# Kernel tuning notes

Hardware: AMD Instinct MI355X
Metric: run time of the kernel (lower is better)

The kernel has to match this reference:

```python
import jax, jax.numpy as jnp
import numpy as np

N, L, H, E, FE = 32, 128, 16, 256, 4  # batch, seq_len, heads, embed_size, forward_expansion
EPS = 1e-5
NEG_SLOPE = 0.01


def _mask_positions(qe):
    # zero entries where j < L-1-i (torch: triu(ones,1).flip(1) == 1)
    Ld = qe.shape[-1]
    i = jnp.arange(Ld)[:, None]
    j = jnp.arange(Ld)[None, :]
    return jnp.where(j >= (Ld - 1 - i), qe, jnp.zeros((), qe.dtype))


def _skew(qe):
    # pad last dim on the left, reinterpret, drop first row -> relative skew
    n, h, Ld, _ = qe.shape
    p = jnp.pad(qe, ((0, 0), (0, 0), (0, 0), (1, 0)))
    return p.reshape(n, h, Ld + 1, Ld)[:, :, 1:, :]


def _batchnorm(x, gamma, beta):
    # BatchNorm1d(C=L*H) over (N, C, E): normalize over batch and embed dims
    mean = jnp.mean(x, axis=(0, 2), keepdims=True)
    var = jnp.var(x, axis=(0, 2), keepdims=True)
    return (x - mean) * jax.lax.rsqrt(var + EPS) * gamma[None, :, None] + beta[None, :, None]


def _leaky(x):
    return jnp.where(x >= 0, x, NEG_SLOPE * x)


def setup_inputs() -> dict:
    key = jax.random.key(0)
    ks = jax.random.split(key, 16)
    s_e = 1.0 / np.sqrt(E)
    d = {
        "x": jax.random.normal(ks[0], (N, L * H, E, 1), dtype=jnp.float32),
        "Wq": jax.random.normal(ks[1], (E, E), dtype=jnp.float32) * s_e,
        "bq": jnp.zeros((E,), jnp.float32),
        "Wk": jax.random.normal(ks[2], (E, E), dtype=jnp.float32) * s_e,
        "bk": jnp.zeros((E,), jnp.float32),
        "Wv": jax.random.normal(ks[3], (E, E), dtype=jnp.float32) * s_e,
        "bv": jnp.zeros((E,), jnp.float32),
        "Erel": jax.random.normal(ks[4], (H, L, E), dtype=jnp.float32),
        "Wo": jax.random.normal(ks[5], (E, E), dtype=jnp.float32) * s_e,
        "bo": jnp.zeros((E,), jnp.float32),
        "g1": jnp.ones((L * H,), jnp.float32),
        "be1": jnp.zeros((L * H,), jnp.float32),
        "g2": jnp.ones((L * H,), jnp.float32),
        "be2": jnp.zeros((L * H,), jnp.float32),
        "W1": jax.random.normal(ks[6], (E, FE * E), dtype=jnp.float32) * s_e,
        "b1": jnp.zeros((FE * E,), jnp.float32),
        "W2": jax.random.normal(ks[7], (FE * E, E), dtype=jnp.float32) * (1.0 / np.sqrt(FE * E)),
        "b2": jnp.zeros((E,), jnp.float32),
        "Wenc": jax.random.normal(ks[8], (E, E), dtype=jnp.float32) * s_e,
        "benc": jnp.zeros((E,), jnp.float32),
    }
    return d


def reference(x, Wq, bq, Wk, bk, Wv, bv, Erel, Wo, bo, g1, be1, g2, be2, W1, b1, W2, b2, Wenc, benc):
    xs = x[:, :, :, 0]  # (N, L*H, E)
    q = (xs @ Wq + bq).reshape(N, L, H, E)
    k = (xs @ Wk + bk).reshape(N, L, H, E)
    v = (xs @ Wv + bv).reshape(N, L, H, E)
    # relative-position skew term (Music-Transformer style)
    QE = jnp.einsum('nlhe,hme->nhlm', q, Erel)       # (N,H,L,L)
    S = _skew(_mask_positions(QE))                   # (N,H,L,L)
    qk = jnp.einsum('nqhe,nkhe->nhqk', q, k)         # (N,H,L,L)
    att = jax.nn.softmax(qk / jnp.sqrt(jnp.float32(E)), axis=-1) + S
    z = jnp.einsum('nhql,nlhe->nqhe', att, v).reshape(N, L * H, E)
    z = z @ Wo + bo
    h1 = _batchnorm(z + xs, g1, be1)
    ff = _leaky(h1 @ W1 + b1) @ W2 + b2
    out = _batchnorm(ff + h1, g2, be2)
    return out @ Wenc + benc
```

## Files before the change

### kernel.cpp

```cpp
#include <hip/hip_runtime.h>
#include <hip/hip_bf16.h>

using u16 = unsigned short;
typedef __attribute__((ext_vector_type(8))) short bf16x8;
typedef __attribute__((ext_vector_type(4))) float f32x4;

static constexpr float EPS_ = 1e-5f;
static constexpr float NEG_ = 0.01f;

__device__ __forceinline__ float bf2f(u16 u) { return __uint_as_float(((unsigned)u) << 16); }
__device__ __forceinline__ u16 f2bf(float f) {
    union { __hip_bfloat16 h; u16 u; } c; c.h = __float2bfloat16(f); return c.u;
}

#define MFMA16(a, b, c) __builtin_amdgcn_mfma_f32_16x16x32_bf16(a, b, c, 0, 0, 0)

__device__ __forceinline__ void gload16(const u16* g, u16* l) {
    __builtin_amdgcn_global_load_lds(
        (__attribute__((address_space(1))) void*)(u16*)g,
        (__attribute__((address_space(3))) void*)l, 16, 0, 0);
}

__device__ __forceinline__ int xswz(int nwg) {
    const int b = blockIdx.x;
    return (b & 7) * (nwg >> 3) + (b >> 3);
}

template<int K>
__device__ __forceinline__ void core256(
    const u16* __restrict__ Ag, int lda,
    const u16* __restrict__ Bg, int ldb,
    u16* SH, f32x4 acc[8][4])
{
    const int tid = threadIdx.x;
    const int w = tid >> 6, lane = tid & 63;
    const int g = lane >> 4, r = lane & 15;
    const int wr = w >> 2, wc = w & 3;
    const int gx = (g ^ ((r >> 1) & 3)) * 8;
    constexpr int NT = K / 32;

    #pragma unroll
    for (int i = 0; i < 8; i++)
        #pragma unroll
        for (int j = 0; j < 4; j++)
            acc[i][j] = (f32x4){0.f, 0.f, 0.f, 0.f};

    auto stage = [&](int buf, int kt, int rnd) {
        const int part = rnd & 1, isB = rnd >> 1;
        const int u = part * 512 + tid;
        const int row = u >> 2;
        const int sc = (u & 3) ^ ((row >> 1) & 3);
        const u16* src = (isB ? Bg + (size_t)row * ldb : Ag + (size_t)row * lda)
                         + kt + sc * 8;
        gload16(src, SH + buf * 16384 + isB * 8192 + u * 8);
    };

    #pragma unroll
    for (int rnd = 0; rnd < 4; ++rnd) stage(0, 0, rnd);
    asm volatile("s_waitcnt vmcnt(0)" ::: "memory");
    __builtin_amdgcn_s_barrier();
    __builtin_amdgcn_sched_barrier(0);

    for (int t = 0; t < NT; ++t) {
        const int buf = t & 1;
        const u16* Ab = SH + buf * 16384;
        const u16* Bb = Ab + 8192;
        const bool pf = (t + 1 < NT);

        if (pf) { stage(buf ^ 1, (t + 1) * 32, 0); stage(buf ^ 1, (t + 1) * 32, 1); }
        bf16x8 bfr[4], af[4];
        #pragma unroll
        for (int fn = 0; fn < 4; ++fn)
            bfr[fn] = *(const bf16x8*)(Bb + (wc * 64 + fn * 16 + r) * 32 + gx);
        #pragma unroll
        for (int f = 0; f < 4; ++f)
            af[f] = *(const bf16x8*)(Ab + (wr * 128 + f * 16 + r) * 32 + gx);
        __builtin_amdgcn_s_setprio(1);
        #pragma unroll
        for (int f = 0; f < 4; ++f)
            #pragma unroll
            for (int fn = 0; fn < 4; ++fn)
                acc[f][fn] = MFMA16(af[f], bfr[fn], acc[f][fn]);
        __builtin_amdgcn_s_setprio(0);

        if (pf) { stage(buf ^ 1, (t + 1) * 32, 2); stage(buf ^ 1, (t + 1) * 32, 3); }
        #pragma unroll
        for (int f = 0; f < 4; ++f)
            af[f] = *(const bf16x8*)(Ab + (wr * 128 + 64 + f * 16 + r) * 32 + gx);
        __builtin_amdgcn_s_setprio(1);
        #pragma unroll
        for (int f = 0; f < 4; ++f)
            #pragma unroll
            for (int fn = 0; fn < 4; ++fn)
                acc[4 + f][fn] = MFMA16(af[f], bfr[fn], acc[4 + f][fn]);
        __builtin_amdgcn_s_setprio(0);

        asm volatile("s_waitcnt vmcnt(0)" ::: "memory");
        __builtin_amdgcn_s_barrier();
        __builtin_amdgcn_sched_barrier(0);
    }
}

template<int K, int NN, int MODE>
__global__ __launch_bounds__(512, 2) void gemm256_k(
    const u16* __restrict__ A, const u16* __restrict__ Bt,
    const float* __restrict__ bias, const u16* __restrict__ res,
    const float2* __restrict__ rp, const float* __restrict__ cs,
    void* __restrict__ outv)
{
    __shared__ __align__(16) u16 SH[36864];
    constexpr int NB = NN / 256;
    const int f = xswz(256 * NB);
    const int m0 = (f / NB) * 256, n0 = (f % NB) * 256;

    f32x4 acc[8][4];
    core256<K>(A + (size_t)m0 * K, K, Bt + (size_t)n0 * K, K, SH, acc);

    const int tid = threadIdx.x;
    const int w = tid >> 6, lane = tid & 63;
    const int g = lane >> 4, r = lane & 15;
    const int wr = w >> 2, wc = w & 3;

    __syncthreads();

    if constexpr (MODE == 3) {
        float* SHf = (float*)SH;
        float* out = (float*)outv;
        #pragma unroll
        for (int q = 0; q < 4; ++q) {
            if (wr == (q >> 1)) {
                const int fmB = (q & 1) * 4;
                #pragma unroll
                for (int fi = 0; fi < 4; ++fi) {
                    #pragma unroll
                    for (int fn = 0; fn < 4; ++fn) {
                        const int col = wc * 64 + fn * 16 + r;
                        const float bv = bias[n0 + col], cv = cs[n0 + col];
                        #pragma unroll
                        for (int reg = 0; reg < 4; ++reg) {
                            const int rl = fi * 16 + g * 4 + reg;
                            const int m = m0 + q * 64 + rl;
                            const float2 pp = rp[m & 2047];
                            SHf[rl * 260 + col] =
                                pp.x * acc[fmB + fi][fn][reg] + pp.y * cv + bv;
                        }
                    }
                }
            }
            __builtin_amdgcn_s_barrier();
            #pragma unroll
            for (int p = 0; p < 8; ++p) {
                const int id = p * 512 + tid;
                const int rl = id >> 6, c4 = id & 63;
                const float4 v = *(const float4*)(SHf + rl * 260 + c4 * 4);
                *(float4*)(out + (size_t)(m0 + q * 64 + rl) * 256 + c4 * 4) = v;
            }
            __builtin_amdgcn_s_barrier();
        }
        return;
    }

    u16* out = (u16*)outv;
    #pragma unroll
    for (int h = 0; h < 2; ++h) {
        if (wr == h) {
            #pragma unroll
            for (int fm = 0; fm < 8; ++fm)
                #pragma unroll
                for (int fn = 0; fn < 4; ++fn) {
                    const int col = wc * 64 + fn * 16 + r;
                    const float bv = bias[n0 + col];
                    #pragma unroll
                    for (int reg = 0; reg < 4; ++reg) {
                        const int rl = fm * 16 + g * 4 + reg;
                        float v = acc[fm][fn][reg];
                        if constexpr (MODE == 1) {
                            const float2 pp = rp[(m0 + h * 128 + rl) & 2047];
                            v = pp.x * v + pp.y * cs[n0 + col] + bv;
                            v = v >= 0.f ? v : NEG_ * v;
                        } else {
                            v += bv;
                        }
                        SH[rl * 264 + col] = f2bf(v);
                    }
                }
        }
        __builtin_amdgcn_s_barrier();
        #pragma unroll
        for (int p = 0; p < 8; ++p) {
            const int ck = p * 512 + tid;
            const int rl = ck >> 5, cc = ck & 31;
            const int m = m0 + h * 128 + rl;
            bf16x8 v = *(const bf16x8*)(SH + rl * 264 + cc * 8);
            if constexpr (MODE == 0) {
                const bf16x8 rv = *(const bf16x8*)(res + (size_t)m * NN + n0 + cc * 8);
                #pragma unroll
                for (int j = 0; j < 8; ++j)
                    v[j] = (short)f2bf(bf2f((u16)v[j]) + bf2f((u16)rv[j]));
            }
            if constexpr (MODE == 2) {
                const float2 pp = rp[m & 2047];
                const bf16x8 rv = *(const bf16x8*)(res + (size_t)m * NN + n0 + cc * 8);
                #pragma unroll
                for (int j = 0; j < 8; ++j)
                    v[j] = (short)f2bf(bf2f((u16)v[j]) + pp.x * bf2f((u16)rv[j]) + pp.y);
            }
            *(bf16x8*)(out + (size_t)m * NN + n0 + cc * 8) = v;
        }
        __builtin_amdgcn_s_barrier();
    }
}

__global__ __launch_bounds__(512, 2) void qkv256_k(
    const u16* __restrict__ xbf, const u16* __restrict__ Wqkvt,
    const float* __restrict__ bq, const float* __restrict__ bk,
    const float* __restrict__ bv,
    u16* __restrict__ qo, u16* __restrict__ ko, u16* __restrict__ vo)
{
    __shared__ __align__(16) u16 SH[36864];
    const int f = xswz(768);
    const int m0 = (f / 3) * 256;
    const int which = f % 3;
    const float* bias = which == 0 ? bq : (which == 1 ? bk : bv);

    f32x4 acc[8][4];
    core256<256>(xbf + (size_t)m0 * 256, 256,
                 Wqkvt + (size_t)which * 65536, 256, SH, acc);

    const int tid = threadIdx.x;
    const int w = tid >> 6, lane = tid & 63;
    const int g = lane >> 4, r = lane & 15;
    const int wr = w >> 2, wc = w & 3;
    const int nn = m0 >> 11;

    __syncthreads();
    if (which < 2) {
        u16* out = which == 0 ? qo : ko;
        #pragma unroll
        for (int h = 0; h < 2; ++h) {
            if (wr == h) {
                #pragma unroll
                for (int fm = 0; fm < 8; ++fm)
                    #pragma unroll
                    for (int fn = 0; fn < 4; ++fn) {
                        const int col = wc * 64 + fn * 16 + r;
                        const float bv4 = bias[col];
                        #pragma unroll
                        for (int reg = 0; reg < 4; ++reg) {
                            const int rl = fm * 16 + g * 4 + reg;
                            SH[rl * 264 + col] = f2bf(acc[fm][fn][reg] + bv4);
                        }
                    }
            }
            __builtin_amdgcn_s_barrier();
            #pragma unroll
            for (int p = 0; p < 8; ++p) {
                const int ck = p * 512 + tid;
                const int rl = ck >> 5, cc = ck & 31;
                const int m = m0 + h * 128 + rl;
                const int l = (m & 2047) >> 4, hh = m & 15;
                const bf16x8 v = *(const bf16x8*)(SH + rl * 264 + cc * 8);
                *(bf16x8*)(out + ((size_t)(nn * 16 + hh) * 128 + l) * 256 + cc * 8) = v;
            }
            __builtin_amdgcn_s_barrier();
        }
    } else {
        #pragma unroll
        for (int h = 0; h < 2; ++h) {
            if (wr == h) {
                #pragma unroll
                for (int fm = 0; fm < 8; ++fm)
                    #pragma unroll
                    for (int fn = 0; fn < 4; ++fn) {
                        const int col = wc * 64 + fn * 16 + r;
                        const float bv4 = bias[col];
                        #pragma unroll
                        for (int reg = 0; reg < 4; ++reg) {
                            const int rl = fm * 16 + g * 4 + reg;
                            SH[col * 136 + ((rl & 15) * 8 | (rl >> 4))] =
                                f2bf(acc[fm][fn][reg] + bv4);
                        }
                    }
            }
            __builtin_amdgcn_s_barrier();
            const int l0 = ((m0 + h * 128) & 2047) >> 4;
            #pragma unroll
            for (int p = 0; p < 8; ++p) {
                const int ck = p * 512 + tid;
                const int e = ck >> 4, hh = ck & 15;
                const bf16x8 v = *(const bf16x8*)(SH + e * 136 + hh * 8);
                *(bf16x8*)(vo + ((size_t)(nn * 16 + hh) * 256 + e) * 128 + l0) = v;
            }
            __builtin_amdgcn_s_barrier();
        }
    }
}

__device__ __forceinline__ void lds_core(
    const u16* __restrict__ Ag, int lda,
    const u16* __restrict__ Bg, int ldb, int K,
    u16* As, u16* Bs, f32x4 acc[4][4])
{
    const int tid = threadIdx.x;
    const int w = tid >> 6, lane = tid & 63;
    const int g = lane >> 4, r = lane & 15;
    const int wm = (w >> 1) * 64, wn = (w & 1) * 64;
    const int rx = r & 7;

    for (int kt = 0; kt < K; kt += 64) {
        #pragma unroll
        for (int j = 0; j < 4; j++) {
            const int ubase = (w * 4 + j) * 64;
            const int u = ubase + lane;
            const int row = u >> 3;
            const int cb = ((u & 7) ^ (row & 7)) * 8;
            gload16(Ag + (size_t)row * lda + kt + cb, As + ubase * 8);
            gload16(Bg + (size_t)row * ldb + kt + cb, Bs + ubase * 8);
        }
        __syncthreads();
        #pragma unroll
        for (int kk = 0; kk < 2; kk++) {
            const int co = ((kk * 4 + g) ^ rx) * 8;
            bf16x8 af[4], bfr[4];
            #pragma unroll
            for (int f = 0; f < 4; f++) {
                af[f]  = *(const bf16x8*)(As + (wm + f * 16 + r) * 64 + co);
                bfr[f] = *(const bf16x8*)(Bs + (wn + f * 16 + r) * 64 + co);
            }
            #pragma unroll
            for (int i = 0; i < 4; i++)
                #pragma unroll
                for (int j = 0; j < 4; j++)
                    acc[i][j] = MFMA16(af[i], bfr[j], acc[i][j]);
        }
        __syncthreads();
    }
}

template<typename OutF>
__device__ __forceinline__ void epi_store128(
    u16* Cs, f32x4 (&acc)[4][4], float scale, OutF outp)
{
    const int tid = threadIdx.x;
    const int w = tid >> 6, lane = tid & 63;
    const int g = lane >> 4, r = lane & 15;
    const int mb = (w >> 1) * 64, nb = (w & 1) * 64;

    #pragma unroll
    for (int fn = 0; fn < 4; fn++) {
        const int col = nb + fn * 16 + r;
        #pragma unroll
        for (int fm = 0; fm < 4; fm++)
            #pragma unroll
            for (int reg = 0; reg < 4; reg++) {
                const int row = mb + fm * 16 + g * 4 + reg;
                Cs[row * 136 + col] = f2bf(acc[fm][fn][reg] * scale);
            }
    }
    __syncthreads();
    #pragma unroll
    for (int p = 0; p < 8; p++) {
        const int ck = p * 256 + tid;
        const int row = ck >> 4, cc = ck & 15;
        const bf16x8 v = *(const bf16x8*)(Cs + row * 136 + cc * 8);
        *(bf16x8*)outp(row, cc) = v;
    }
}

__global__ __launch_bounds__(256) void qkqe_k(
    const u16* __restrict__ q, const u16* __restrict__ kc,
    const u16* __restrict__ erel, u16* __restrict__ out)
{
    __shared__ __align__(16) u16 SH[17408];
    u16* As = SH; u16* Bs = SH + 8192;
    const int f = xswz(1024);
    const int b = f >> 1, h = b & 15;
    const int n0 = (f & 1) * 128;
    const u16* Ag = q + (size_t)b * 128 * 256;
    const u16* Bg = (n0 == 0) ? (kc + (size_t)b * 128 * 256)
                              : (erel + (size_t)h * 128 * 256);

    f32x4 acc[4][4];
    #pragma unroll
    for (int i = 0; i < 4; i++)
        #pragma unroll
        for (int j = 0; j < 4; j++) acc[i][j] = (f32x4){0.f,0.f,0.f,0.f};
    lds_core(Ag, 256, Bg, 256, 256, As, Bs, acc);

    const float scale = (n0 == 0) ? 0.0625f : 1.0f;
    __syncthreads();
    epi_store128(SH, acc, scale,
        [&](int row, int cc) -> u16* {
            return out + ((size_t)b * 128 + row) * 256 + n0 + cc * 8;
        });
}

__global__ __launch_bounds__(256) void softmax_k(
    const u16* __restrict__ qk, u16* __restrict__ att)
{
    const int r = blockIdx.x * 4 + (threadIdx.x >> 6);
    const int lane = threadIdx.x & 63;
    const int i = r & 127;
    const u16* row = qk + (size_t)r * 256;
    const float x0 = bf2f(row[lane]), x1 = bf2f(row[lane + 64]);
    float mx = fmaxf(x0, x1);
    #pragma unroll
    for (int o = 32; o; o >>= 1) mx = fmaxf(mx, __shfl_xor(mx, o));
    const float e0 = __expf(x0 - mx), e1 = __expf(x1 - mx);
    float s = e0 + e1;
    #pragma unroll
    for (int o = 32; o; o >>= 1) s += __shfl_xor(s, o);
    const float rinv = 1.0f / s;
    const float s0 = (lane <= i) ? bf2f(row[128 + 127 - i + lane]) : 0.f;
    const float s1 = (lane + 64 <= i) ? bf2f(row[128 + 127 - i + lane + 64]) : 0.f;
    att[(size_t)r * 128 + lane] = f2bf(e0 * rinv + s0);
    att[(size_t)r * 128 + lane + 64] = f2bf(e1 * rinv + s1);
}

__global__ __launch_bounds__(256) void av_k(
    const u16* __restrict__ att, const u16* __restrict__ vT,
    u16* __restrict__ zc)
{
    __shared__ __align__(16) u16 SH[17408];
    u16* As = SH; u16* Bs = SH + 8192;
    const int f = xswz(1024);
    const int b = f >> 1;
    const int n0 = (f & 1) * 128;
    const u16* Ag = att + (size_t)b * 128 * 128;
    const u16* Bg = vT + (size_t)b * 256 * 128 + (size_t)n0 * 128;

    f32x4 acc[4][4];
    #pragma unroll
    for (int i = 0; i < 4; i++)
        #pragma unroll
        for (int j = 0; j < 4; j++) acc[i][j] = (f32x4){0.f,0.f,0.f,0.f};
    lds_core(Ag, 128, Bg, 128, 128, As, Bs, acc);

    const int nn = b >> 4, hh = b & 15;
    __syncthreads();
    epi_store128(SH, acc, 1.f,
        [&](int row, int cc) -> u16* {
            return zc + ((size_t)(nn * 2048 + row * 16 + hh)) * 256 + n0 + cc * 8;
        });
}

__global__ __launch_bounds__(256) void cvt_k(const float* __restrict__ in,
                                             u16* __restrict__ out) {
    const size_t i8 = ((size_t)blockIdx.x * 256 + threadIdx.x) * 8;
    const float4 lo = *(const float4*)(in + i8);
    const float4 hi = *(const float4*)(in + i8 + 4);
    ushort4 o0, o1;
    o0.x = f2bf(lo.x); o0.y = f2bf(lo.y); o0.z = f2bf(lo.z); o0.w = f2bf(lo.w);
    o1.x = f2bf(hi.x); o1.y = f2bf(hi.y); o1.z = f2bf(hi.z); o1.w = f2bf(hi.w);
    *(ushort4*)(out + i8) = o0;
    *(ushort4*)(out + i8 + 4) = o1;
}

__global__ __launch_bounds__(256) void prep_w_k(
    const float* __restrict__ Wq, const float* __restrict__ Wk,
    const float* __restrict__ Wv, const float* __restrict__ Wo,
    const float* __restrict__ Wenc, const float* __restrict__ W1,
    const float* __restrict__ W2, const float* __restrict__ Erel,
    u16* __restrict__ Wqkvt, u16* __restrict__ Wot, u16* __restrict__ Wenct,
    u16* __restrict__ W1t, u16* __restrict__ W2t, u16* __restrict__ Erelb,
    float* __restrict__ cs1, float* __restrict__ csE)
{
    const int bid = blockIdx.x, tid = threadIdx.x;
    if (bid < 1280) {
        const int jb = bid >> 8;
        const int t = ((bid & 255) << 8) | tid;
        const int n = t >> 8, k = t & 255;
        const float* src = jb == 0 ? Wq : jb == 1 ? Wk : jb == 2 ? Wv
                         : jb == 3 ? Wo : Wenc;
        const u16 v = f2bf(src[(k << 8) + n]);
        if (jb < 3)       Wqkvt[jb * 65536 + t] = v;
        else if (jb == 3) Wot[t] = v;
        else              Wenct[t] = v;
    } else if (bid < 2304) {
        const int t = ((bid - 1280) << 8) | tid;
        const int n = t >> 8, k = t & 255;
        W1t[t] = f2bf(W1[(k << 10) + n]);
    } else if (bid < 3328) {
        const int t = ((bid - 2304) << 8) | tid;
        const int n = t >> 10, k = t & 1023;
        W2t[t] = f2bf(W2[(k << 8) + n]);
    } else if (bid < 5376) {
        const int t = ((bid - 3328) << 8) | tid;
        Erelb[t] = f2bf(Erel[t]);
    } else {
        const int n = (bid - 5376) * 256 + tid;
        if (n < 1024) {
            float s = 0.f;
            for (int k = 0; k < 256; ++k) s += bf2f(f2bf(W1[(size_t)k * 1024 + n]));
            cs1[n] = s;
        } else {
            const int n2 = n - 1024;
            float s = 0.f;
            for (int k = 0; k < 256; ++k) s += bf2f(f2bf(Wenc[(size_t)k * 256 + n2]));
            csE[n2] = s;
        }
    }
}

__global__ __launch_bounds__(256) void bnstats_k(
    const u16* __restrict__ x, const float* __restrict__ g,
    const float* __restrict__ be, float2* __restrict__ params)
{
    const int c = blockIdx.x, tid = threadIdx.x;
    float s = 0.f, s2 = 0.f;
    #pragma unroll 4
    for (int n = 0; n < 32; n++) {
        const float v = bf2f(x[((size_t)n * 2048 + c) * 256 + tid]);
        s += v; s2 += v * v;
    }
    #pragma unroll
    for (int o = 32; o; o >>= 1) { s += __shfl_xor(s, o); s2 += __shfl_xor(s2, o); }
    __shared__ float rs[4], rs2[4];
    const int w = tid >> 6;
    if ((tid & 63) == 0) { rs[w] = s; rs2[w] = s2; }
    __syncthreads();
    if (tid == 0) {
        s  = rs[0] + rs[1] + rs[2] + rs[3];
        s2 = rs2[0] + rs2[1] + rs2[2] + rs2[3];
        const float mean = s / 8192.f;
        const float var = s2 / 8192.f - mean * mean;
        const float a = g[c] * rsqrtf(var + EPS_);
        params[c] = make_float2(a, be[c] - mean * a);
    }
}

extern "C" void kernel_launch(void* const* d_in, const int* in_sizes, int n_in,
                              void* d_out, int out_size, void* d_ws, size_t ws_size,
                              hipStream_t stream)
{
    const float* x    = (const float*)d_in[0];
    const float* Wq   = (const float*)d_in[1];
    const float* bq   = (const float*)d_in[2];
    const float* Wk   = (const float*)d_in[3];
    const float* bk   = (const float*)d_in[4];
    const float* Wv   = (const float*)d_in[5];
    const float* bv   = (const float*)d_in[6];
    const float* Erel = (const float*)d_in[7];
    const float* Wo   = (const float*)d_in[8];
    const float* bo   = (const float*)d_in[9];
    const float* g1   = (const float*)d_in[10];
    const float* be1  = (const float*)d_in[11];
    const float* g2   = (const float*)d_in[12];
    const float* be2  = (const float*)d_in[13];
    const float* W1   = (const float*)d_in[14];
    const float* b1   = (const float*)d_in[15];
    const float* W2   = (const float*)d_in[16];
    const float* b2   = (const float*)d_in[17];
    const float* Wenc = (const float*)d_in[18];
    const float* benc = (const float*)d_in[19];

    char* ws = (char*)d_ws;
    const size_t MB = 1ull << 20;
    const size_t KB = 1024;
    u16* xbf   = (u16*)(ws + 0 * MB);
    u16* h2pre = (u16*)(ws + 32 * MB);
    u16* qb    = (u16*)(ws + 32 * MB);
    u16* kb    = (u16*)(ws + 64 * MB);
    u16* vT    = (u16*)(ws + 96 * MB);
    u16* qkb   = (u16*)(ws + 128 * MB);
    u16* attb  = (u16*)(ws + 160 * MB);
    u16* ff1   = (u16*)(ws + 64 * MB);
    u16* zc    = (u16*)(ws + 176 * MB);
    u16* h1pre = (u16*)(ws + 208 * MB);
    u16* Wqkvt = (u16*)(ws + 240 * MB);
    u16* Wot   = (u16*)(ws + 240 * MB + 512 * KB);
    u16* Wenct = (u16*)(ws + 240 * MB + 640 * KB);
    u16* W1t   = (u16*)(ws + 240 * MB + 768 * KB);
    u16* W2t   = (u16*)(ws + 240 * MB + 1280 * KB);
    u16* Erelb = (u16*)(ws + 240 * MB + 1792 * KB);
    float2* p1 = (float2*)(ws + 243 * MB);
    float2* p2 = (float2*)(ws + 243 * MB + 16 * KB);
    float* cs1 = (float*)(ws + 243 * MB + 32 * KB);
    float* csE = (float*)(ws + 243 * MB + 40 * KB);

    const dim3 b256(256), b512(512);

    cvt_k<<<dim3(8192), b256, 0, stream>>>(x, xbf);
    prep_w_k<<<dim3(5381), b256, 0, stream>>>(Wq, Wk, Wv, Wo, Wenc, W1, W2, Erel,
                                              Wqkvt, Wot, Wenct, W1t, W2t, Erelb,
                                              cs1, csE);

    qkv256_k<<<dim3(768), b512, 0, stream>>>(xbf, Wqkvt, bq, bk, bv, qb, kb, vT);
    qkqe_k<<<dim3(1024), b256, 0, stream>>>(qb, kb, Erelb, qkb);
    softmax_k<<<dim3(16384), b256, 0, stream>>>(qkb, attb);
    av_k<<<dim3(1024), b256, 0, stream>>>(attb, vT, zc);
    gemm256_k<256, 256, 0><<<dim3(256), b512, 0, stream>>>(
        zc, Wot, bo, xbf, nullptr, nullptr, h1pre);

    bnstats_k<<<dim3(2048), b256, 0, stream>>>(h1pre, g1, be1, p1);

    gemm256_k<256, 1024, 1><<<dim3(1024), b512, 0, stream>>>(
        h1pre, W1t, b1, nullptr, p1, cs1, ff1);
    gemm256_k<1024, 256, 2><<<dim3(256), b512, 0, stream>>>(
        ff1, W2t, b2, h1pre, p1, nullptr, h2pre);

    bnstats_k<<<dim3(2048), b256, 0, stream>>>(h2pre, g2, be2, p2);
    gemm256_k<256, 256, 3><<<dim3(256), b512, 0, stream>>>(
        h2pre, Wenct, benc, nullptr, p2, csE, (float*)d_out);
}
```

Before: 337.1 us.

## Deepen GEMM core pipeline to 64-wide K steps with two-stage prefetch

The shared 256x256 GEMM core now processes K in 64-element steps split into two 32-wide halves. Loads for the next halves are issued two stages ahead, and partial vmcnt waits replace the full drain before each barrier. The LDS swizzle changes to match the new layout. LDS per block grows to 128 KB and the launch bounds drop the two-blocks-per-CU hint, so occupancy likely falls to one 512-thread block per CU in exchange for more latency hiding.

```diff
diff --git a/kernel.cpp b/kernel.cpp
--- a/kernel.cpp
+++ b/kernel.cpp
@@ -36,8 +36,8 @@
     const int w = tid >> 6, lane = tid & 63;
     const int g = lane >> 4, r = lane & 15;
     const int wr = w >> 2, wc = w & 3;
-    const int gx = (g ^ ((r >> 1) & 3)) * 8;
-    constexpr int NT = K / 32;
+    const int gx = (g ^ (r & 3)) * 8;
+    constexpr int NT = K / 64;
 
     #pragma unroll
     for (int i = 0; i < 8; i++)
@@ -45,36 +45,46 @@
         for (int j = 0; j < 4; j++)
             acc[i][j] = (f32x4){0.f, 0.f, 0.f, 0.f};
 
-    auto stage = [&](int buf, int kt, int rnd) {
-        const int part = rnd & 1, isB = rnd >> 1;
-        const int u = part * 512 + tid;
-        const int row = u >> 2;
-        const int sc = (u & 3) ^ ((row >> 1) & 3);
-        const u16* src = (isB ? Bg + (size_t)row * ldb : Ag + (size_t)row * lda)
-                         + kt + sc * 8;
-        gload16(src, SH + buf * 16384 + isB * 8192 + u * 8);
+    auto stage_half = [&](int Tt, int which) {
+        const int isB = which & 1, kh = which >> 1;
+        const int d2 = Tt & 1;
+        u16* base = SH + (size_t)((d2 * 2 + isB) * 2 + kh) * 8192;
+        const u16* gbase = isB ? Bg : Ag;
+        const int ld = isB ? ldb : lda;
+        const int kt = Tt * 64 + kh * 32;
+        #pragma unroll
+        for (int part = 0; part < 2; ++part) {
+            const int u = part * 512 + tid;
+            const int row = u >> 2;
+            const int gslot = (u & 3) ^ (row & 3);
+            gload16(gbase + (size_t)row * ld + kt + gslot * 8, base + u * 8);
+        }
     };
 
-    #pragma unroll
-    for (int rnd = 0; rnd < 4; ++rnd) stage(0, 0, rnd);
-    asm volatile("s_waitcnt vmcnt(0)" ::: "memory");
-    __builtin_amdgcn_s_barrier();
-    __builtin_amdgcn_sched_barrier(0);
+    stage_half(0, 0); stage_half(0, 1); stage_half(0, 2); stage_half(0, 3);
+    stage_half(1, 0); stage_half(1, 1);
 
     for (int t = 0; t < NT; ++t) {
-        const int buf = t & 1;
-        const u16* Ab = SH + buf * 16384;
-        const u16* Bb = Ab + 8192;
-        const bool pf = (t + 1 < NT);
-
-        if (pf) { stage(buf ^ 1, (t + 1) * 32, 0); stage(buf ^ 1, (t + 1) * 32, 1); }
-        bf16x8 bfr[4], af[4];
+        const int d = t & 1;
+        const u16* Ak0 = SH + (size_t)(d * 4 + 0) * 8192;
+        const u16* Ak1 = SH + (size_t)(d * 4 + 1) * 8192;
+        const u16* Bk0 = SH + (size_t)(d * 4 + 2) * 8192;
+        const u16* Bk1 = SH + (size_t)(d * 4 + 3) * 8192;
+        const bool pf1 = (t + 1 < NT), pf2 = (t + 2 < NT);
+
+        if (pf1) asm volatile("s_waitcnt vmcnt(8)" ::: "memory");
+        else     asm volatile("s_waitcnt vmcnt(4)" ::: "memory");
+        __builtin_amdgcn_s_barrier();
+        __builtin_amdgcn_sched_barrier(0);
+
+        bf16x8 af[4], bfr[4];
         #pragma unroll
         for (int fn = 0; fn < 4; ++fn)
-            bfr[fn] = *(const bf16x8*)(Bb + (wc * 64 + fn * 16 + r) * 32 + gx);
-        #pragma unroll
-        for (int f = 0; f < 4; ++f)
-            af[f] = *(const bf16x8*)(Ab + (wr * 128 + f * 16 + r) * 32 + gx);
+            bfr[fn] = *(const bf16x8*)(Bk0 + (wc * 64 + fn * 16 + r) * 32 + gx);
+        #pragma unroll
+        for (int f = 0; f < 4; ++f)
+            af[f] = *(const bf16x8*)(Ak0 + (wr * 128 + f * 16 + r) * 32 + gx);
+        if (pf1) stage_half(t + 1, 2);
         __builtin_amdgcn_s_setprio(1);
         #pragma unroll
         for (int f = 0; f < 4; ++f)
@@ -82,11 +92,10 @@
             for (int fn = 0; fn < 4; ++fn)
                 acc[f][fn] = MFMA16(af[f], bfr[fn], acc[f][fn]);
         __builtin_amdgcn_s_setprio(0);
-
-        if (pf) { stage(buf ^ 1, (t + 1) * 32, 2); stage(buf ^ 1, (t + 1) * 32, 3); }
-        #pragma unroll
-        for (int f = 0; f < 4; ++f)
-            af[f] = *(const bf16x8*)(Ab + (wr * 128 + 64 + f * 16 + r) * 32 + gx);
+        #pragma unroll
+        for (int f = 0; f < 4; ++f)
+            af[f] = *(const bf16x8*)(Ak0 + (wr * 128 + 64 + f * 16 + r) * 32 + gx);
+        if (pf1) stage_half(t + 1, 3);
         __builtin_amdgcn_s_setprio(1);
         #pragma unroll
         for (int f = 0; f < 4; ++f)
@@ -95,20 +104,47 @@
                 acc[4 + f][fn] = MFMA16(af[f], bfr[fn], acc[4 + f][fn]);
         __builtin_amdgcn_s_setprio(0);
 
-        asm volatile("s_waitcnt vmcnt(0)" ::: "memory");
+        if (pf1) asm volatile("s_waitcnt vmcnt(8)" ::: "memory");
+        else     asm volatile("s_waitcnt vmcnt(0)" ::: "memory");
         __builtin_amdgcn_s_barrier();
         __builtin_amdgcn_sched_barrier(0);
+
+        #pragma unroll
+        for (int fn = 0; fn < 4; ++fn)
+            bfr[fn] = *(const bf16x8*)(Bk1 + (wc * 64 + fn * 16 + r) * 32 + gx);
+        #pragma unroll
+        for (int f = 0; f < 4; ++f)
+            af[f] = *(const bf16x8*)(Ak1 + (wr * 128 + f * 16 + r) * 32 + gx);
+        if (pf2) stage_half(t + 2, 0);
+        __builtin_amdgcn_s_setprio(1);
+        #pragma unroll
+        for (int f = 0; f < 4; ++f)
+            #pragma unroll
+            for (int fn = 0; fn < 4; ++fn)
+                acc[f][fn] = MFMA16(af[f], bfr[fn], acc[f][fn]);
+        __builtin_amdgcn_s_setprio(0);
+        #pragma unroll
+        for (int f = 0; f < 4; ++f)
+            af[f] = *(const bf16x8*)(Ak1 + (wr * 128 + 64 + f * 16 + r) * 32 + gx);
+        if (pf2) stage_half(t + 2, 1);
+        __builtin_amdgcn_s_setprio(1);
+        #pragma unroll
+        for (int f = 0; f < 4; ++f)
+            #pragma unroll
+            for (int fn = 0; fn < 4; ++fn)
+                acc[4 + f][fn] = MFMA16(af[f], bfr[fn], acc[4 + f][fn]);
+        __builtin_amdgcn_s_setprio(0);
     }
 }
 
 template<int K, int NN, int MODE>
-__global__ __launch_bounds__(512, 2) void gemm256_k(
+__global__ __launch_bounds__(512) void gemm256_k(
     const u16* __restrict__ A, const u16* __restrict__ Bt,
     const float* __restrict__ bias, const u16* __restrict__ res,
     const float2* __restrict__ rp, const float* __restrict__ cs,
     void* __restrict__ outv)
 {
-    __shared__ __align__(16) u16 SH[36864];
+    __shared__ __align__(16) u16 SH[65536];
     constexpr int NB = NN / 256;
     const int f = xswz(256 * NB);
     const int m0 = (f / NB) * 256, n0 = (f % NB) * 256;
@@ -211,13 +247,13 @@
     }
 }
 
-__global__ __launch_bounds__(512, 2) void qkv256_k(
+__global__ __launch_bounds__(512) void qkv256_k(
     const u16* __restrict__ xbf, const u16* __restrict__ Wqkvt,
     const float* __restrict__ bq, const float* __restrict__ bk,
     const float* __restrict__ bv,
     u16* __restrict__ qo, u16* __restrict__ ko, u16* __restrict__ vo)
 {
-    __shared__ __align__(16) u16 SH[36864];
+    __shared__ __align__(16) u16 SH[65536];
     const int f = xswz(768);
     const int m0 = (f / 3) * 256;
     const int which = f % 3;
```

Result: no change. 332.3 us (-1.4%).
